# Kernel optimization log

Measured on AMD Instinct MI355X. Metric: run time of the kernel, lower is better.

The kernel has to match this reference:

```python
import jax, jax.numpy as jnp
import numpy as np

N, E, F, H, C = 50000, 800000, 128, 128, 64
NEG_SLOPE = 0.2


def setup_inputs() -> dict:
    key = jax.random.key(0)
    ks = jax.random.split(key, 12)
    s = 1.0 / np.sqrt(H)
    return {
        "x": jax.random.normal(ks[0], (N, F), jnp.float32),
        "edge_index": jax.random.randint(ks[1], (2, E), 0, N, jnp.int64),
        "W1": jax.random.normal(ks[2], (F, H), jnp.float32) * s,
        "b1": jnp.zeros((H,), jnp.float32),
        "Wg1": jax.random.normal(ks[3], (H, H), jnp.float32) * s,
        "asrc1": jax.random.normal(ks[4], (H,), jnp.float32) * s,
        "adst1": jax.random.normal(ks[5], (H,), jnp.float32) * s,
        "bg1": jnp.zeros((H,), jnp.float32),
        "W2": jax.random.normal(ks[6], (H, H), jnp.float32) * s,
        "b2": jnp.zeros((H,), jnp.float32),
        "Wg2": jax.random.normal(ks[7], (H, H), jnp.float32) * s,
        "asrc2": jax.random.normal(ks[8], (H,), jnp.float32) * s,
        "adst2": jax.random.normal(ks[9], (H,), jnp.float32) * s,
        "bg2": jnp.zeros((H,), jnp.float32),
        "Wo": jax.random.normal(ks[10], (H, C), jnp.float32) * s,
        "bo": jnp.zeros((C,), jnp.float32),
    }


def _gcn(x, src, dst, n, W, b):
    # PyG GCNConv: add self-loops (done by caller), symmetric normalization
    xw = x @ W
    deg = jax.ops.segment_sum(jnp.ones(src.shape[0], xw.dtype), dst, num_segments=n)
    inv = jax.lax.rsqrt(deg)  # deg >= 1 due to self-loops
    coef = inv[src] * inv[dst]
    return jax.ops.segment_sum(coef[:, None] * xw[src], dst, num_segments=n) + b


def _gat(x, src, dst, n, W, a_s, a_d, b):
    # PyG GATConv, heads=1: segment softmax over destination nodes
    xw = x @ W
    e = jax.nn.leaky_relu((xw @ a_s)[src] + (xw @ a_d)[dst], NEG_SLOPE)
    m = jax.ops.segment_max(e, dst, num_segments=n)
    ex = jnp.exp(e - m[dst])
    denom = jax.ops.segment_sum(ex, dst, num_segments=n)
    alpha = ex / denom[dst]
    return jax.ops.segment_sum(alpha[:, None] * xw[src], dst, num_segments=n) + b


def reference(x, edge_index, W1, b1, Wg1, asrc1, adst1, bg1,
              W2, b2, Wg2, asrc2, adst2, bg2, Wo, bo):
    n = x.shape[0]
    loops = jnp.arange(n, dtype=edge_index.dtype)
    src = jnp.concatenate([edge_index[0], loops])
    dst = jnp.concatenate([edge_index[1], loops])

    h = jax.nn.relu(_gcn(x, src, dst, n, W1, b1))
    h = jax.nn.relu(_gat(h, src, dst, n, Wg1, asrc1, adst1, bg1))
    h = jax.nn.relu(_gcn(h, src, dst, n, W2, b2))
    h = jax.nn.relu(_gat(h, src, dst, n, Wg2, asrc2, adst2, bg2))
    z = h @ Wo + bo
    return (h, z)
```

## Files before the change

kernel.cpp:

```cpp
#include <hip/hip_runtime.h>
#include <hip/hip_bf16.h>
#include <hip/hip_fp16.h>


#define WAVE 64
#define BK 256
#define CHUNK 4096

typedef _Float16 f16x8 __attribute__((ext_vector_type(8)));
typedef float f32x4 __attribute__((ext_vector_type(4)));

__global__ void k_zero_i32(int* __restrict__ p, int n) {
    int i = blockIdx.x * 256 + threadIdx.x;
    if (i < n) p[i] = 0;
}


__global__ __launch_bounds__(256) void k_bhist(
    const int* __restrict__ ei, int* __restrict__ bcnt,
    int E, int Et, int nbuck) {
    __shared__ int hist[256];
    int tid = threadIdx.x;
    if (tid < nbuck) hist[tid] = 0;
    __syncthreads();
    for (int e = blockIdx.x * 256 + tid; e < Et; e += gridDim.x * 256) {
        int d = (e < E) ? ei[E + e] : (e - E);
        atomicAdd(&hist[d >> 8], 1);
    }
    __syncthreads();
    if (tid < nbuck && hist[tid] > 0) atomicAdd(&bcnt[tid], hist[tid]);
}

__global__ void k_bscan(const int* __restrict__ bcnt, int* __restrict__ bbase,
                        int* __restrict__ bcur, int nbuck) {
    __shared__ int tmp[256];
    int tid = threadIdx.x;
    int v = (tid < nbuck) ? bcnt[tid] : 0;
    tmp[tid] = v;
    __syncthreads();
    for (int off = 1; off < 256; off <<= 1) {
        int t = (tid >= off) ? tmp[tid - off] : 0;
        __syncthreads();
        tmp[tid] += t;
        __syncthreads();
    }
    if (tid < nbuck) {
        int excl = tmp[tid] - v;
        bbase[tid] = excl;
        bcur[tid] = excl;
        if (tid == nbuck - 1) bbase[nbuck] = tmp[tid];
    }
}

__global__ __launch_bounds__(256) void k_bscatter(
    const int* __restrict__ ei, int* __restrict__ bcur,
    int2* __restrict__ ebuf, int E, int Et, int nbuck) {
    __shared__ int hist[256];
    __shared__ int base[256];
    __shared__ int off[256];
    constexpr int PT = CHUNK / 256;
    int tid = threadIdx.x;
    int cb = blockIdx.x * CHUNK;
    if (tid < nbuck) { hist[tid] = 0; off[tid] = 0; }
    __syncthreads();

    int sv[PT], dv[PT];
#pragma unroll
    for (int i = 0; i < PT; ++i) {
        int e = cb + i * 256 + tid;
        int s = 0, d = -1;
        if (e < Et) {
            if (e < E) { s = ei[e]; d = ei[E + e]; }
            else       { s = d = e - E; }
            atomicAdd(&hist[d >> 8], 1);
        }
        sv[i] = s; dv[i] = d;
    }
    __syncthreads();
    if (tid < nbuck && hist[tid] > 0)
        base[tid] = atomicAdd(&bcur[tid], hist[tid]);
    __syncthreads();
#pragma unroll
    for (int i = 0; i < PT; ++i) {
        if (dv[i] >= 0) {
            int b = dv[i] >> 8;
            int pos = base[b] + atomicAdd(&off[b], 1);
            ebuf[pos] = make_int2(sv[i], dv[i]);
        }
    }
}

__global__ __launch_bounds__(256) void k_csr(
    const int2* __restrict__ ebuf, const int* __restrict__ bbase,
    int* __restrict__ rowp, float* __restrict__ inv, int* __restrict__ esrc,
    int Nn, int Et) {
    __shared__ int hist[256];
    __shared__ int scan[256];
    __shared__ int cur[256];
    int tid = threadIdx.x;
    int b = blockIdx.x;
    int bb = bbase[b], cnt = bbase[b + 1] - bb;
    hist[tid] = 0;
    __syncthreads();
    for (int t = tid; t < cnt; t += 256)
        atomicAdd(&hist[ebuf[bb + t].y & 255], 1);
    __syncthreads();
    int v = hist[tid];
    scan[tid] = v;
    __syncthreads();
    for (int o = 1; o < 256; o <<= 1) {
        int t = (tid >= o) ? scan[tid - o] : 0;
        __syncthreads();
        scan[tid] += t;
        __syncthreads();
    }
    int excl = scan[tid] - v;
    int node = b * BK + tid;
    if (node < Nn) {
        rowp[node] = bb + excl;
        inv[node] = rsqrtf((float)v);
    }
    cur[tid] = excl;
    if (b == 0 && tid == 0) rowp[Nn] = Et;
    __syncthreads();
    for (int t = tid; t < cnt; t += 256) {
        int2 e = ebuf[bb + t];
        int pos = bb + atomicAdd(&cur[e.y & 255], 1);
        esrc[pos] = e.x;
    }
}


__global__ void k_wcvt(const float* __restrict__ W1, const float* __restrict__ Wg1,
                       const float* __restrict__ W2, const float* __restrict__ Wg2,
                       const float* __restrict__ Wo, __half* __restrict__ Wt) {
    int i = blockIdx.x * 256 + threadIdx.x;
    if (i < 65536) {
        int w = i >> 14;
        int j = i & 16383;
        int n = j >> 7, k = j & 127;
        const float* W = (w == 0) ? W1 : (w == 1) ? Wg1 : (w == 2) ? W2 : Wg2;
        Wt[i] = __float2half(W[k * 128 + n]);
    } else if (i < 73728) {
        int j = i - 65536;
        int n = j >> 7, k = j & 127;
        Wt[65536 + j] = __float2half(Wo[k * 64 + n]);
    }
}


template <int NC, typename OT>
__global__ __launch_bounds__(256) void gemm_mfma(
    const float* __restrict__ A, const __half* __restrict__ Wt,
    const float* __restrict__ bias, OT* __restrict__ out,
    const float* __restrict__ asrc, const float* __restrict__ adst,
    float* __restrict__ alS, float* __restrict__ alD, int M) {
    constexpr int NT = NC / 16;
    constexpr int LDW = 136;
    __shared__ _Float16 Wl[NC * LDW];
    const int tid = threadIdx.x;
    const int wv = tid >> 6, lane = tid & 63;
    const int m16 = lane & 15, quad = lane >> 4;

    for (int i = tid; i < NC * 16; i += 256) {
        int r = i >> 4, c8 = i & 15;
        *(float4*)(&Wl[r * LDW + c8 * 8]) =
            *(const float4*)((const _Float16*)Wt + r * 128 + c8 * 8);
    }
    __syncthreads();

    const int row0 = blockIdx.x * 128 + wv * 32;

    f16x8 af[2][4];
#pragma unroll
    for (int mt = 0; mt < 2; ++mt) {
        int row = row0 + mt * 16 + m16;
        if (row > M - 1) row = M - 1;
        const float* ap = A + (size_t)row * 128 + quad * 8;
#pragma unroll
        for (int ks = 0; ks < 4; ++ks) {
            float4 lo = *(const float4*)(ap + ks * 32);
            float4 hi = *(const float4*)(ap + ks * 32 + 4);
            f16x8 v;
            v[0] = (_Float16)lo.x; v[1] = (_Float16)lo.y;
            v[2] = (_Float16)lo.z; v[3] = (_Float16)lo.w;
            v[4] = (_Float16)hi.x; v[5] = (_Float16)hi.y;
            v[6] = (_Float16)hi.z; v[7] = (_Float16)hi.w;
            af[mt][ks] = v;
        }
    }

    f32x4 acc[2][NT];
#pragma unroll
    for (int mt = 0; mt < 2; ++mt)
#pragma unroll
        for (int nt = 0; nt < NT; ++nt)
            acc[mt][nt] = (f32x4){0.f, 0.f, 0.f, 0.f};

#pragma unroll
    for (int ks = 0; ks < 4; ++ks) {
#pragma unroll
        for (int nt = 0; nt < NT; ++nt) {
            f16x8 bf = *(const f16x8*)(&Wl[(nt * 16 + m16) * LDW + ks * 32 + quad * 8]);
            acc[0][nt] = __builtin_amdgcn_mfma_f32_16x16x32_f16(
                af[0][ks], bf, acc[0][nt], 0, 0, 0);
            acc[1][nt] = __builtin_amdgcn_mfma_f32_16x16x32_f16(
                af[1][ks], bf, acc[1][nt], 0, 0, 0);
        }
    }

    if (asrc) {
        float sa[NT], da[NT];
#pragma unroll
        for (int nt = 0; nt < NT; ++nt) {
            sa[nt] = asrc[nt * 16 + m16];
            da[nt] = adst[nt * 16 + m16];
        }
#pragma unroll
        for (int mt = 0; mt < 2; ++mt) {
#pragma unroll
            for (int r = 0; r < 4; ++r) {
                float s = 0.f, d = 0.f;
#pragma unroll
                for (int nt = 0; nt < NT; ++nt) {
                    s = fmaf(acc[mt][nt][r], sa[nt], s);
                    d = fmaf(acc[mt][nt][r], da[nt], d);
                }
#pragma unroll
                for (int off = 8; off > 0; off >>= 1) {
                    s += __shfl_xor(s, off);
                    d += __shfl_xor(d, off);
                }
                int row = row0 + mt * 16 + quad * 4 + r;
                if (m16 == 0 && row < M) { alS[row] = s; alD[row] = d; }
            }
        }
    }

#pragma unroll
    for (int mt = 0; mt < 2; ++mt) {
#pragma unroll
        for (int nt = 0; nt < NT; ++nt) {
#pragma unroll
            for (int r = 0; r < 4; ++r) {
                int row = row0 + mt * 16 + quad * 4 + r;
                if (row < M) {
                    float v = acc[mt][nt][r];
                    int col = nt * 16 + m16;
                    if constexpr (sizeof(OT) == 2) {
                        ((__half*)out)[(size_t)row * NC + col] = __float2half(v);
                    } else {
                        ((float*)out)[(size_t)row * NC + col] = v + bias[col];
                    }
                }
            }
        }
    }
}


__device__ __forceinline__ void gather_accum_h(
    const __half* __restrict__ xw, int q, int g, int cnt, int sid, float wgt,
    float acc[8]) {
    for (int base = 0; base < cnt; base += 32) {
        int c = cnt - base;
        float4 x[8];
        float w[8];
#pragma unroll
        for (int u = 0; u < 8; ++u) {
            if (u * 4 < c) {
                int idx = base + 4 * u + g;
                int s = __shfl(sid, idx);
                w[u] = __shfl(wgt, idx);
                x[u] = *(const float4*)(xw + (size_t)s * 128 + q * 8);
            }
        }
#pragma unroll
        for (int u = 0; u < 8; ++u) {
            if (u * 4 < c) {
                const __half2* h2 = (const __half2*)&x[u];
#pragma unroll
                for (int i = 0; i < 4; ++i) {
                    float2 cc = __half22float2(h2[i]);
                    acc[2 * i]     = fmaf(w[u], cc.x, acc[2 * i]);
                    acc[2 * i + 1] = fmaf(w[u], cc.y, acc[2 * i + 1]);
                }
            }
        }
    }
}

__device__ __forceinline__ void finish_store_q(
    float acc[8], const float* __restrict__ bias, float* __restrict__ out,
    int n, int q, int g) {
#pragma unroll
    for (int i = 0; i < 8; ++i) {
        acc[i] += __shfl_xor(acc[i], 16);
        acc[i] += __shfl_xor(acc[i], 32);
    }
    if (g == 0) {
        float4 b0 = ((const float4*)bias)[q * 2];
        float4 b1 = ((const float4*)bias)[q * 2 + 1];
        float4 r0, r1;
        r0.x = fmaxf(acc[0] + b0.x, 0.f);
        r0.y = fmaxf(acc[1] + b0.y, 0.f);
        r0.z = fmaxf(acc[2] + b0.z, 0.f);
        r0.w = fmaxf(acc[3] + b0.w, 0.f);
        r1.x = fmaxf(acc[4] + b1.x, 0.f);
        r1.y = fmaxf(acc[5] + b1.y, 0.f);
        r1.z = fmaxf(acc[6] + b1.z, 0.f);
        r1.w = fmaxf(acc[7] + b1.w, 0.f);
        float4* orow = (float4*)(out + (size_t)n * 128);
        orow[q * 2]     = r0;
        orow[q * 2 + 1] = r1;
    }
}

__global__ __launch_bounds__(256) void k_gcn_agg(
    const __half* __restrict__ xw, const int* __restrict__ rowp,
    const int* __restrict__ esrc, const float* __restrict__ inv,
    const float* __restrict__ bias, float* __restrict__ out, int Nn) {
    int gid = blockIdx.x * 256 + threadIdx.x;
    int n = gid >> 6, lane = gid & 63;
    if (n >= Nn) return;
    int q = lane & 15, g = lane >> 4;
    int beg = rowp[n], end = rowp[n + 1];
    float invd = inv[n];
    float acc[8] = {0.f, 0.f, 0.f, 0.f, 0.f, 0.f, 0.f, 0.f};
    for (int base = beg; base < end; base += WAVE) {
        int e = base + lane;
        bool valid = (e < end);
        int sid = valid ? esrc[e] : 0;
        float c = valid ? invd * inv[sid] : 0.f;
        gather_accum_h(xw, q, g, min(WAVE, end - base), sid, c, acc);
    }
    finish_store_q(acc, bias, out, n, q, g);
}

__global__ __launch_bounds__(256) void k_gat_agg(
    const __half* __restrict__ xw, const int* __restrict__ rowp,
    const int* __restrict__ esrc, const float* __restrict__ as_,
    const float* __restrict__ ad_, const float* __restrict__ bias,
    float* __restrict__ out, int Nn) {
    int gid = blockIdx.x * 256 + threadIdx.x;
    int n = gid >> 6, lane = gid & 63;
    if (n >= Nn) return;
    int q = lane & 15, g = lane >> 4;
    int beg = rowp[n], end = rowp[n + 1];
    int deg = end - beg;
    float adn = ad_[n];
    float acc[8] = {0.f, 0.f, 0.f, 0.f, 0.f, 0.f, 0.f, 0.f};

    if (deg <= WAVE) {
        bool valid = (lane < deg);
        int sid = 0;
        float v = -1e30f;
        if (valid) {
            sid = esrc[beg + lane];
            float t = as_[sid] + adn;
            v = (t > 0.f) ? t : 0.2f * t;
        }
        float m = v;
#pragma unroll
        for (int off = 32; off > 0; off >>= 1) m = fmaxf(m, __shfl_xor(m, off));
        float ex = valid ? __expf(v - m) : 0.f;
        float ssum = ex;
#pragma unroll
        for (int off = 32; off > 0; off >>= 1) ssum += __shfl_xor(ssum, off);
        float wgt = ex * (1.f / ssum);
        gather_accum_h(xw, q, g, deg, sid, wgt, acc);
    } else {
        float m = -1e30f, ssum = 0.f;
        for (int e = beg + lane; e < end; e += WAVE) {
            float v = as_[esrc[e]] + adn;
            v = (v > 0.f) ? v : 0.2f * v;
            float mn = fmaxf(m, v);
            ssum = ssum * __expf(m - mn) + __expf(v - mn);
            m = mn;
        }
#pragma unroll
        for (int off = 32; off > 0; off >>= 1) {
            float mo = __shfl_xor(m, off);
            float so = __shfl_xor(ssum, off);
            float mn = fmaxf(m, mo);
            ssum = ssum * __expf(m - mn) + so * __expf(mo - mn);
            m = mn;
        }
        float rden = 1.f / ssum;
        for (int base = beg; base < end; base += WAVE) {
            int e = base + lane;
            bool valid = (e < end);
            int sid = valid ? esrc[e] : 0;
            float wgt = 0.f;
            if (valid) {
                float v = as_[sid] + adn;
                v = (v > 0.f) ? v : 0.2f * v;
                wgt = __expf(v - m) * rden;
            }
            gather_accum_h(xw, q, g, min(WAVE, end - base), sid, wgt, acc);
        }
    }
    finish_store_q(acc, bias, out, n, q, g);
}


extern "C" void kernel_launch(void* const* d_in, const int* in_sizes, int n_in,
                              void* d_out, int out_size, void* d_ws, size_t ws_size,
                              hipStream_t stream) {
    const float* x   = (const float*)d_in[0];
    const int*   ei  = (const int*)d_in[1];
    const float* W1  = (const float*)d_in[2];
    const float* b1  = (const float*)d_in[3];
    const float* Wg1 = (const float*)d_in[4];
    const float* as1 = (const float*)d_in[5];
    const float* ad1 = (const float*)d_in[6];
    const float* bg1 = (const float*)d_in[7];
    const float* W2  = (const float*)d_in[8];
    const float* b2  = (const float*)d_in[9];
    const float* Wg2 = (const float*)d_in[10];
    const float* as2 = (const float*)d_in[11];
    const float* ad2 = (const float*)d_in[12];
    const float* bg2 = (const float*)d_in[13];
    const float* Wo  = (const float*)d_in[14];
    const float* bo  = (const float*)d_in[15];

    const int Nn = in_sizes[0] / 128;
    const int E  = in_sizes[1] / 2;
    const int Et = E + Nn;
    const int H  = 128;
    const int nbuck = (Nn + BK - 1) / BK;

    float* outH = (float*)d_out;
    float* outZ = outH + (size_t)Nn * H;

    char* p = (char*)d_ws;
    auto carve = [&](size_t bytes) {
        char* r = p;
        p += (bytes + 255) & ~(size_t)255;
        return r;
    };
    __half* bufA = (__half*)carve((size_t)Nn * H * sizeof(__half));
    __half* Wt   = (__half*)carve((size_t)73728 * sizeof(__half));
    float* alS   = (float*)carve((size_t)Nn * sizeof(float));
    float* alD   = (float*)carve((size_t)Nn * sizeof(float));
    float* inv   = (float*)carve((size_t)Nn * sizeof(float));
    int*   rowp  = (int*)carve((size_t)(Nn + 1) * sizeof(int));
    int*   esrc  = (int*)carve((size_t)Et * sizeof(int));
    int2*  ebuf  = (int2*)carve((size_t)Et * sizeof(int2));
    int*   bcnt  = (int*)carve((size_t)nbuck * sizeof(int));
    int*   bbase = (int*)carve((size_t)(nbuck + 1) * sizeof(int));
    int*   bcur  = (int*)carve((size_t)nbuck * sizeof(int));
    (void)ws_size; (void)n_in; (void)out_size;

    const int aggBlocks = (Nn * WAVE + 255) / 256;
    const int gemmB = (Nn + 127) / 128;
    const int scatB = (Et + CHUNK - 1) / CHUNK;

    k_zero_i32<<<1, 256, 0, stream>>>(bcnt, nbuck);
    k_bhist<<<104, 256, 0, stream>>>(ei, bcnt, E, Et, nbuck);
    k_bscan<<<1, 256, 0, stream>>>(bcnt, bbase, bcur, nbuck);
    k_bscatter<<<scatB, 256, 0, stream>>>(ei, bcur, ebuf, E, Et, nbuck);
    k_csr<<<nbuck, 256, 0, stream>>>(ebuf, bbase, rowp, inv, esrc, Nn, Et);
    k_wcvt<<<288, 256, 0, stream>>>(W1, Wg1, W2, Wg2, Wo, Wt);

    gemm_mfma<128, __half><<<gemmB, 256, 0, stream>>>(
        x, Wt, nullptr, bufA, nullptr, nullptr, nullptr, nullptr, Nn);
    k_gcn_agg<<<aggBlocks, 256, 0, stream>>>(bufA, rowp, esrc, inv, b1, outH, Nn);

    gemm_mfma<128, __half><<<gemmB, 256, 0, stream>>>(
        outH, Wt + 16384, nullptr, bufA, as1, ad1, alS, alD, Nn);
    k_gat_agg<<<aggBlocks, 256, 0, stream>>>(bufA, rowp, esrc, alS, alD, bg1, outH, Nn);

    gemm_mfma<128, __half><<<gemmB, 256, 0, stream>>>(
        outH, Wt + 32768, nullptr, bufA, nullptr, nullptr, nullptr, nullptr, Nn);
    k_gcn_agg<<<aggBlocks, 256, 0, stream>>>(bufA, rowp, esrc, inv, b2, outH, Nn);

    gemm_mfma<128, __half><<<gemmB, 256, 0, stream>>>(
        outH, Wt + 49152, nullptr, bufA, as2, ad2, alS, alD, Nn);
    k_gat_agg<<<aggBlocks, 256, 0, stream>>>(bufA, rowp, esrc, alS, alD, bg2, outH, Nn);

    gemm_mfma<64, float><<<gemmB, 256, 0, stream>>>(
        outH, Wt + 65536, bo, outZ, nullptr, nullptr, nullptr, nullptr, Nn);
}
```

Measured before the change: 382.8 us.

## Pre-swizzle weights into MFMA fragment order and halve GEMM rows per block

The weight conversion kernel now writes the transposed fp16 weights directly in per-lane MFMA B-fragment order, so the GEMM loads each fragment with one contiguous 16-byte LDS read and needs no padded stride. Each wave now handles one 16-row M tile instead of two, and each block covers 64 rows, so the grid doubles. This aims to cut LDS bank conflicts and register pressure and to raise occupancy, in exchange for loading the weight tile into LDS twice as often per output row.

```diff
diff --git a/kernel.cpp b/kernel.cpp
--- a/kernel.cpp
+++ b/kernel.cpp
@@ -138,12 +138,16 @@
     if (i < 65536) {
         int w = i >> 14;
         int j = i & 16383;
-        int n = j >> 7, k = j & 127;
+        int nt = j >> 11, ks = (j >> 9) & 3, lane = (j >> 3) & 63, jj = j & 7;
+        int n = nt * 16 + (lane & 15);
+        int k = ks * 32 + (lane >> 4) * 8 + jj;
         const float* W = (w == 0) ? W1 : (w == 1) ? Wg1 : (w == 2) ? W2 : Wg2;
         Wt[i] = __float2half(W[k * 128 + n]);
     } else if (i < 73728) {
         int j = i - 65536;
-        int n = j >> 7, k = j & 127;
+        int nt = j >> 11, ks = (j >> 9) & 3, lane = (j >> 3) & 63, jj = j & 7;
+        int n = nt * 16 + (lane & 15);
+        int k = ks * 32 + (lane >> 4) * 8 + jj;
         Wt[65536 + j] = __float2half(Wo[k * 64 + n]);
     }
 }
@@ -156,25 +160,21 @@
     const float* __restrict__ asrc, const float* __restrict__ adst,
     float* __restrict__ alS, float* __restrict__ alD, int M) {
     constexpr int NT = NC / 16;
-    constexpr int LDW = 136;
-    __shared__ _Float16 Wl[NC * LDW];
+    __shared__ f16x8 Wl[NC * 16];
     const int tid = threadIdx.x;
     const int wv = tid >> 6, lane = tid & 63;
     const int m16 = lane & 15, quad = lane >> 4;
 
-    for (int i = tid; i < NC * 16; i += 256) {
-        int r = i >> 4, c8 = i & 15;
-        *(float4*)(&Wl[r * LDW + c8 * 8]) =
-            *(const float4*)((const _Float16*)Wt + r * 128 + c8 * 8);
-    }
-    __syncthreads();
-
-    const int row0 = blockIdx.x * 128 + wv * 32;
-
-    f16x8 af[2][4];
-#pragma unroll
-    for (int mt = 0; mt < 2; ++mt) {
-        int row = row0 + mt * 16 + m16;
+#pragma unroll
+    for (int i = tid; i < NC * 16; i += 256)
+        Wl[i] = ((const f16x8*)Wt)[i];
+    __syncthreads();
+
+    const int row0 = blockIdx.x * 64 + wv * 16;
+
+    f16x8 af[4];
+    {
+        int row = row0 + m16;
         if (row > M - 1) row = M - 1;
         const float* ap = A + (size_t)row * 128 + quad * 8;
 #pragma unroll
@@ -186,26 +186,22 @@
             v[2] = (_Float16)lo.z; v[3] = (_Float16)lo.w;
             v[4] = (_Float16)hi.x; v[5] = (_Float16)hi.y;
             v[6] = (_Float16)hi.z; v[7] = (_Float16)hi.w;
-            af[mt][ks] = v;
-        }
-    }
-
-    f32x4 acc[2][NT];
-#pragma unroll
-    for (int mt = 0; mt < 2; ++mt)
-#pragma unroll
-        for (int nt = 0; nt < NT; ++nt)
-            acc[mt][nt] = (f32x4){0.f, 0.f, 0.f, 0.f};
+            af[ks] = v;
+        }
+    }
+
+    f32x4 acc[NT];
+#pragma unroll
+    for (int nt = 0; nt < NT; ++nt)
+        acc[nt] = (f32x4){0.f, 0.f, 0.f, 0.f};
 
 #pragma unroll
     for (int ks = 0; ks < 4; ++ks) {
 #pragma unroll
         for (int nt = 0; nt < NT; ++nt) {
-            f16x8 bf = *(const f16x8*)(&Wl[(nt * 16 + m16) * LDW + ks * 32 + quad * 8]);
-            acc[0][nt] = __builtin_amdgcn_mfma_f32_16x16x32_f16(
-                af[0][ks], bf, acc[0][nt], 0, 0, 0);
-            acc[1][nt] = __builtin_amdgcn_mfma_f32_16x16x32_f16(
-                af[1][ks], bf, acc[1][nt], 0, 0, 0);
+            f16x8 bf = Wl[(nt * 4 + ks) * 64 + lane];
+            acc[nt] = __builtin_amdgcn_mfma_f32_16x16x32_f16(
+                af[ks], bf, acc[nt], 0, 0, 0);
         }
     }
 
@@ -217,41 +213,35 @@
             da[nt] = adst[nt * 16 + m16];
         }
 #pragma unroll
-        for (int mt = 0; mt < 2; ++mt) {
-#pragma unroll
-            for (int r = 0; r < 4; ++r) {
-                float s = 0.f, d = 0.f;
-#pragma unroll
-                for (int nt = 0; nt < NT; ++nt) {
-                    s = fmaf(acc[mt][nt][r], sa[nt], s);
-                    d = fmaf(acc[mt][nt][r], da[nt], d);
-                }
-#pragma unroll
-                for (int off = 8; off > 0; off >>= 1) {
-                    s += __shfl_xor(s, off);
-                    d += __shfl_xor(d, off);
-                }
-                int row = row0 + mt * 16 + quad * 4 + r;
-                if (m16 == 0 && row < M) { alS[row] = s; alD[row] = d; }
-            }
-        }
-    }
-
-#pragma unroll
-    for (int mt = 0; mt < 2; ++mt) {
-#pragma unroll
-        for (int nt = 0; nt < NT; ++nt) {
-#pragma unroll
-            for (int r = 0; r < 4; ++r) {
-                int row = row0 + mt * 16 + quad * 4 + r;
-                if (row < M) {
-                    float v = acc[mt][nt][r];
-                    int col = nt * 16 + m16;
-                    if constexpr (sizeof(OT) == 2) {
-                        ((__half*)out)[(size_t)row * NC + col] = __float2half(v);
-                    } else {
-                        ((float*)out)[(size_t)row * NC + col] = v + bias[col];
-                    }
+        for (int r = 0; r < 4; ++r) {
+            float s = 0.f, d = 0.f;
+#pragma unroll
+            for (int nt = 0; nt < NT; ++nt) {
+                s = fmaf(acc[nt][r], sa[nt], s);
+                d = fmaf(acc[nt][r], da[nt], d);
+            }
+#pragma unroll
+            for (int off = 8; off > 0; off >>= 1) {
+                s += __shfl_xor(s, off);
+                d += __shfl_xor(d, off);
+            }
+            int row = row0 + quad * 4 + r;
+            if (m16 == 0 && row < M) { alS[row] = s; alD[row] = d; }
+        }
+    }
+
+#pragma unroll
+    for (int nt = 0; nt < NT; ++nt) {
+#pragma unroll
+        for (int r = 0; r < 4; ++r) {
+            int row = row0 + quad * 4 + r;
+            if (row < M) {
+                float v = acc[nt][r];
+                int col = nt * 16 + m16;
+                if constexpr (sizeof(OT) == 2) {
+                    ((__half*)out)[(size_t)row * NC + col] = __float2half(v);
+                } else {
+                    ((float*)out)[(size_t)row * NC + col] = v + bias[col];
                 }
             }
         }
@@ -453,7 +443,7 @@
     (void)ws_size; (void)n_in; (void)out_size;
 
     const int aggBlocks = (Nn * WAVE + 255) / 256;
-    const int gemmB = (Nn + 127) / 128;
+    const int gemmB = (Nn + 63) / 64;
     const int scatB = (Et + CHUNK - 1) / CHUNK;
 
     k_zero_i32<<<1, 256, 0, stream>>>(bcnt, nbuck);
```

Measured after the change: 378.4 us. No clear change (-1.1%).
